# Optimization experiments

Measured on AMD Instinct MI355X. Metric: run time of the kernel, lower is better.

## Reference

```python
import jax, jax.numpy as jnp
import numpy as np
from jax import lax

# ---- configuration (matches init_kwargs / input_specs) ----
N = 16384          # number of input points
F_IN = 64          # input feature dim
RATIO = 0.25       # fps ratio
M = int(N * RATIO) # number of sampled centers = 4096
RADIUS = 0.2       # radius for neighbor search
K = 64             # max_num_neighbors
F_HID = 64
F_OUT = 128


def _glorot(key, shape):
    fan_in = shape[0]
    return jax.random.normal(key, shape, jnp.float32) / jnp.sqrt(jnp.float32(fan_in))


def setup_inputs() -> dict:
    key = jax.random.key(0)
    ks = jax.random.split(key, 6)
    x = jax.random.normal(ks[0], (N, F_IN), jnp.float32)
    pos = jax.random.normal(ks[1], (N, 3), jnp.float32)
    batch = jnp.zeros((N,), jnp.int32)  # single point cloud
    # PointNet++ SA conv MLP: [F_IN+3 -> 64 -> 64 -> 128]
    W1 = _glorot(ks[2], (F_IN + 3, F_HID))
    b1 = jnp.zeros((F_HID,), jnp.float32)
    W2 = _glorot(ks[3], (F_HID, F_HID))
    b2 = jnp.zeros((F_HID,), jnp.float32)
    W3 = _glorot(ks[4], (F_HID, F_OUT))
    b3 = jnp.zeros((F_OUT,), jnp.float32)
    return {"x": x, "pos": pos, "batch": batch,
            "W1": W1, "b1": b1, "W2": W2, "b2": b2, "W3": W3, "b3": b3}


def fps(pos, m):
    """Farthest point sampling: returns m indices into pos [N,3]."""
    n = pos.shape[0]

    def step(carry, _):
        min_d2, last = carry
        d2 = jnp.sum((pos - pos[last]) ** 2, axis=-1)   # [N]
        min_d2 = jnp.minimum(min_d2, d2)
        nxt = jnp.argmax(min_d2).astype(jnp.int32)
        return (min_d2, nxt), last

    init = (jnp.full((n,), jnp.inf, pos.dtype), jnp.int32(0))
    _, idx = lax.scan(step, init, None, length=m)
    return idx  # [m]


def radius_neighbors(pos, pos_s, batch, batch_s, r, k):
    """For each center, k nearest neighbors within radius r (same batch).
    Returns nbr indices [M,K] and validity mask [M,K]."""
    d2 = jnp.sum((pos_s[:, None, :] - pos[None, :, :]) ** 2, axis=-1)  # [M,N]
    ok = (batch_s[:, None] == batch[None, :]) & (d2 <= r * r)
    score = jnp.where(ok, d2, jnp.inf)
    neg_vals, nbr = lax.top_k(-score, k)                # smallest distances first
    valid = jnp.isfinite(neg_vals)
    return nbr, valid


def reference(x, pos, batch, W1, b1, W2, b2, W3, b3):
    idx = fps(pos, M)                   # [M]
    pos_s = pos[idx]                    # [M,3]
    batch_s = batch[idx]                # [M]
    nbr, valid = radius_neighbors(pos, pos_s, batch, batch_s, RADIUS, K)
    # gather neighbor features and relative positions
    rel = pos[nbr] - pos_s[:, None, :]                      # [M,K,3]
    h = jnp.concatenate([x[nbr], rel], axis=-1)             # [M,K,F_IN+3]
    # per-edge MLP (PointNetConv message)
    h = jax.nn.relu(h @ W1 + b1)
    h = jax.nn.relu(h @ W2 + b2)
    h = jax.nn.relu(h @ W3 + b3)                            # [M,K,F_OUT]
    # max aggregation over valid neighbors (center is always its own neighbor)
    h = jnp.where(valid[..., None], h, -jnp.inf)
    out = jnp.max(h, axis=1)                                # [M,F_OUT]
    return out, pos_s, batch_s
```

## Files before the change

### kernel.cpp

```cpp
#include <hip/hip_runtime.h>

#define N_PTS 16384
#define M_CTR 4096
#define K_NBR 64
#define F_OUT 128
#define CAP   256
#define FS    68
#define NCELL 4096
#define NBKT  512

__device__ __forceinline__ float d2_exact(float ax, float ay, float az,
                                          float bx, float by, float bz) {
  float dx = __fsub_rn(ax, bx);
  float dy = __fsub_rn(ay, by);
  float dz = __fsub_rn(az, bz);
  return __fadd_rn(__fadd_rn(__fmul_rn(dx, dx), __fmul_rn(dy, dy)),
                   __fmul_rn(dz, dz));
}

__device__ __forceinline__ float readlane_f(float v, int ln) {
  return __int_as_float(__builtin_amdgcn_readlane(__float_as_int(v), ln));
}

__device__ __forceinline__ unsigned long long wave_max_u64(unsigned long long v) {
  int lo = (int)(unsigned)v;
  int hi = (int)(unsigned)(v >> 32);
#define DPPSTEP64(ctrl, rm)                                                    \
  {                                                                            \
    int tlo = __builtin_amdgcn_update_dpp(lo, lo, ctrl, rm, 0xf, false);       \
    int thi = __builtin_amdgcn_update_dpp(hi, hi, ctrl, rm, 0xf, false);       \
    unsigned long long cur =                                                   \
        ((unsigned long long)(unsigned)hi << 32) | (unsigned)lo;               \
    unsigned long long oth =                                                   \
        ((unsigned long long)(unsigned)thi << 32) | (unsigned)tlo;             \
    if (oth > cur) { lo = tlo; hi = thi; }                                     \
  }
  DPPSTEP64(0x111, 0xf) DPPSTEP64(0x112, 0xf) DPPSTEP64(0x114, 0xf)
  DPPSTEP64(0x118, 0xf) DPPSTEP64(0x142, 0xa) DPPSTEP64(0x143, 0xc)
#undef DPPSTEP64
  const unsigned rlo = (unsigned)__builtin_amdgcn_readlane(lo, 63);
  const unsigned rhi = (unsigned)__builtin_amdgcn_readlane(hi, 63);
  return ((unsigned long long)rhi << 32) | rlo;
}

__device__ __forceinline__ unsigned long long bucket_bfly_max_u64(
    unsigned long long red) {
#define RORSTEP(ctrl)                                                          \
  {                                                                            \
    int lo = (int)(unsigned)red, hi = (int)(unsigned)(red >> 32);              \
    int tlo = __builtin_amdgcn_update_dpp(lo, lo, ctrl, 0xf, 0xf, false);      \
    int thi = __builtin_amdgcn_update_dpp(hi, hi, ctrl, 0xf, 0xf, false);      \
    unsigned long long o =                                                     \
        ((unsigned long long)(unsigned)thi << 32) | (unsigned)tlo;             \
    if (o > red) red = o;                                                      \
  }
  RORSTEP(0x121) RORSTEP(0x122) RORSTEP(0x124) RORSTEP(0x128)
#undef RORSTEP
  const unsigned olo = (unsigned)__shfl_xor((int)(unsigned)red, 16);
  const unsigned ohi = (unsigned)__shfl_xor((int)(unsigned)(red >> 32), 16);
  const unsigned long long o = ((unsigned long long)ohi << 32) | olo;
  return (o > red) ? o : red;
}

__global__ void __launch_bounds__(1024) prep_bbox_kernel(const float* __restrict__ pos,
                                                         float* __restrict__ bbox,
                                                         int* __restrict__ hist) {
  const int tid = threadIdx.x;
  __shared__ float sred[6][16];
  float mn[3] = {INFINITY, INFINITY, INFINITY};
  float mx[3] = {-INFINITY, -INFINITY, -INFINITY};
  for (int p = tid; p < N_PTS; p += 1024) {
#pragma unroll
    for (int d = 0; d < 3; ++d) {
      float v = pos[3 * p + d];
      mn[d] = fminf(mn[d], v);
      mx[d] = fmaxf(mx[d], v);
    }
  }
#pragma unroll
  for (int off = 32; off > 0; off >>= 1) {
#pragma unroll
    for (int d = 0; d < 3; ++d) {
      mn[d] = fminf(mn[d], __shfl_xor(mn[d], off));
      mx[d] = fmaxf(mx[d], __shfl_xor(mx[d], off));
    }
  }
  if ((tid & 63) == 0) {
    const int w = tid >> 6;
#pragma unroll
    for (int d = 0; d < 3; ++d) { sred[d][w] = mn[d]; sred[3 + d][w] = mx[d]; }
  }
  __syncthreads();
  if (tid == 0) {
#pragma unroll
    for (int d = 0; d < 3; ++d) {
      float a = sred[d][0], b = sred[3 + d][0];
      for (int w = 1; w < 16; ++w) { a = fminf(a, sred[d][w]); b = fmaxf(b, sred[3 + d][w]); }
      bbox[d] = a; bbox[3 + d] = b;
    }
  }
  for (int i = tid; i < NCELL; i += 1024) hist[i] = 0;
}

__device__ __forceinline__ int spread4(int v) {
  return (v & 1) | ((v & 2) << 2) | ((v & 4) << 4) | ((v & 8) << 6);
}

__global__ void __launch_bounds__(256) prep_cell_kernel(const float* __restrict__ pos,
                                                        const float* __restrict__ bbox,
                                                        int* __restrict__ cellid,
                                                        int* __restrict__ hist) {
  const int p = blockIdx.x * 256 + threadIdx.x;
  const float x = pos[3 * p], y = pos[3 * p + 1], z = pos[3 * p + 2];
  const float x0 = bbox[0], y0 = bbox[1], z0 = bbox[2];
  const float sx = 16.0f / fmaxf(bbox[3] - x0, 1e-20f);
  const float sy = 16.0f / fmaxf(bbox[4] - y0, 1e-20f);
  const float sz = 16.0f / fmaxf(bbox[5] - z0, 1e-20f);
  int cx = min(15, (int)((x - x0) * sx));
  int cy = min(15, (int)((y - y0) * sy));
  int cz = min(15, (int)((z - z0) * sz));
  const int c = spread4(cx) | (spread4(cy) << 1) | (spread4(cz) << 2);
  cellid[p] = c;
  atomicAdd(&hist[c], 1);
}

__global__ void __launch_bounds__(1024) prep_scan_kernel(const int* __restrict__ hist,
                                                         int* __restrict__ cursor) {
  __shared__ int tsum[1024];
  const int t = threadIdx.x;
  const int v0 = hist[4 * t + 0], v1 = hist[4 * t + 1];
  const int v2 = hist[4 * t + 2], v3 = hist[4 * t + 3];
  const int s = v0 + v1 + v2 + v3;
  int acc = s;
  tsum[t] = acc;
  __syncthreads();
  for (int off = 1; off < 1024; off <<= 1) {
    int add = (t >= off) ? tsum[t - off] : 0;
    __syncthreads();
    acc += add;
    tsum[t] = acc;
    __syncthreads();
  }
  int base = acc - s;
  cursor[4 * t + 0] = base;
  cursor[4 * t + 1] = base + v0;
  cursor[4 * t + 2] = base + v0 + v1;
  cursor[4 * t + 3] = base + v0 + v1 + v2;
}

__global__ void __launch_bounds__(256) prep_scatter_kernel(const float* __restrict__ pos,
                                                           const int* __restrict__ cellid,
                                                           int* __restrict__ cursor,
                                                           float4* __restrict__ gxyz) {
  const int p = blockIdx.x * 256 + threadIdx.x;
  const int c = cellid[p];
  const int dst = atomicAdd(&cursor[c], 1);
  gxyz[dst] = make_float4(pos[3 * p + 0], pos[3 * p + 1], pos[3 * p + 2],
                          __int_as_float(p));
}

__global__ void __launch_bounds__(64) prep_bktbox_kernel(const float4* __restrict__ gxyz,
                                                         float* __restrict__ gbox) {
  const int lane = threadIdx.x;
  const float4 q = gxyz[blockIdx.x * 64 + lane];
  float mnx = q.x, mxx = q.x, mny = q.y, mxy = q.y, mnz = q.z, mxz = q.z;
#pragma unroll
  for (int off = 16; off > 0; off >>= 1) {
    mnx = fminf(mnx, __shfl_xor(mnx, off)); mxx = fmaxf(mxx, __shfl_xor(mxx, off));
    mny = fminf(mny, __shfl_xor(mny, off)); mxy = fmaxf(mxy, __shfl_xor(mxy, off));
    mnz = fminf(mnz, __shfl_xor(mnz, off)); mxz = fmaxf(mxz, __shfl_xor(mxz, off));
  }
  if ((lane & 31) == 0) {
    const int b = blockIdx.x * 2 + (lane >> 5);
    gbox[b * 8 + 0] = mnx; gbox[b * 8 + 1] = mxx;
    gbox[b * 8 + 2] = mny; gbox[b * 8 + 3] = mxy;
    gbox[b * 8 + 4] = mnz; gbox[b * 8 + 5] = mxz;
    gbox[b * 8 + 6] = 0.0f; gbox[b * 8 + 7] = 0.0f;
  }
}

__global__ void __launch_bounds__(512) fps_bucket_kernel(
    const float* __restrict__ pos, const float4* __restrict__ gxyz,
    const float* __restrict__ gbox,
    int* __restrict__ idx_out, float* __restrict__ pos_s_out,
    float* __restrict__ batch_s_out) {
  __shared__ float s_md[N_PTS];
  __shared__ unsigned long long s_pk[NBKT];
  __shared__ float4 s_wxyz[NBKT];
  __shared__ int s_wl[NBKT];
  __shared__ int s_cnt[2];
  __shared__ int s_sidx[M_CTR];
  const int tid = threadIdx.x;
  const int lane = tid & 63, wave = tid >> 6;

  for (int i = tid; i < N_PTS; i += 512) s_md[i] = INFINITY;
  const float bx0 = gbox[tid * 8 + 0], bx1 = gbox[tid * 8 + 1];
  const float by0 = gbox[tid * 8 + 2], by1 = gbox[tid * 8 + 3];
  const float bz0 = gbox[tid * 8 + 4], bz1 = gbox[tid * 8 + 5];
  unsigned long long mpk = ((unsigned long long)0x7f800000u << 32);
  s_pk[tid] = mpk;
  if (tid < 2) s_cnt[tid] = 0;

  float cxA = pos[0], cyA = pos[1], czA = pos[2];
  int idA = 0;
  float cxB = 0.0f, cyB = 0.0f, czB = 0.0f;
  int idB = 0;
  bool dual = false;
  int t = 0, rc = 0;
  __syncthreads();

  while (true) {
    if (tid == 0) s_sidx[t] = idA;
    ++t;
    if (t >= M_CTR) break;
    if (dual) {
      if (tid == 0) s_sidx[t] = idB;
      ++t;
      if (t >= M_CTR) break;
    }
    const int par = rc & 1;
    ++rc;

    const float rMax = __uint_as_float((unsigned)(mpk >> 32));
    float dxl = fmaxf(fmaxf(bx0 - cxA, cxA - bx1), 0.0f);
    float dyl = fmaxf(fmaxf(by0 - cyA, cyA - by1), 0.0f);
    float dzl = fmaxf(fmaxf(bz0 - czA, czA - bz1), 0.0f);
    bool flag = (dxl * dxl + dyl * dyl + dzl * dzl) * 0.99999f < rMax;
    if (dual) {
      float ex = fmaxf(fmaxf(bx0 - cxB, cxB - bx1), 0.0f);
      float ey = fmaxf(fmaxf(by0 - cyB, cyB - by1), 0.0f);
      float ez = fmaxf(fmaxf(bz0 - czB, czB - bz1), 0.0f);
      flag = flag || ((ex * ex + ey * ey + ez * ez) * 0.99999f < rMax);
    }
    const unsigned long long ball = __ballot(flag);
    int base = 0;
    if (lane == 0) base = atomicAdd(&s_cnt[par], __popcll(ball));
    base = __builtin_amdgcn_readfirstlane(base);
    if (flag) {
      const int pre = __popcll(ball & ((1ull << lane) - 1ull));
      s_wl[base + pre] = tid;
    }
    __syncthreads();
    if (tid == 0) s_cnt[par ^ 1] = 0;

    const int nf = s_cnt[par];
    const int total = nf << 5;
    for (int bi = 0; bi < total; bi += 512) {
      const int idx = bi + tid;
      if (idx < total) {
        const int b = s_wl[idx >> 5];
        const int p = (b << 5) | (idx & 31);
        const float4 q = gxyz[p];
        float nmd = fminf(s_md[p], d2_exact(q.x, q.y, q.z, cxA, cyA, czA));
        if (dual) nmd = fminf(nmd, d2_exact(q.x, q.y, q.z, cxB, cyB, czB));
        s_md[p] = nmd;
        const unsigned long long own =
            ((unsigned long long)__float_as_uint(nmd) << 32) |
            ((unsigned long long)(16383u - (unsigned)__float_as_int(q.w)) << 14) |
            (unsigned)p;
        const unsigned long long red = bucket_bfly_max_u64(own);
        if (own == red) {
          s_pk[b] = red;
          s_wxyz[b] = make_float4(q.x, q.y, q.z, 0.0f);
        }
      }
    }
    __syncthreads();

    unsigned long long vv[8];
    unsigned long long loc = 0ULL;
#pragma unroll
    for (int k = 0; k < 8; ++k) {
      const unsigned long long u = s_pk[(k << 6) | lane];
      vv[k] = u;
      if (k == wave) mpk = u;
      if (u > loc) loc = u;
    }
    const unsigned long long bpk = wave_max_u64(loc);
    idA = 16383 - (int)((bpk >> 14) & 16383u);
    const int posn1 = (int)(bpk & 16383u);
    const int b1 = posn1 >> 5;
    {
      const float4 cq = s_wxyz[b1];
      cxA = cq.x; cyA = cq.y; czA = cq.z;
    }

    unsigned long long loc2 = 0ULL;
#pragma unroll
    for (int k = 0; k < 8; ++k) {
      const int bb = (k << 6) | lane;
      const unsigned long long u = (bb == b1) ? 0ULL : vv[k];
      if (u > loc2) loc2 = u;
    }
    const int pp = (b1 << 5) | (lane & 31);
    const float mdv = s_md[pp];
    const float4 qq = gxyz[pp];
    unsigned long long spk =
        ((unsigned long long)__float_as_uint(mdv) << 32) |
        ((unsigned long long)(16383u - (unsigned)__float_as_int(qq.w)) << 14) |
        (unsigned)pp;
    if (pp == posn1) spk = 0ULL;
    if (spk > loc2) loc2 = spk;
    const unsigned long long Rpk = wave_max_u64(loc2);
    const unsigned hiR = (unsigned)(Rpk >> 32);
    const int posnR = (int)(Rpk & 16383u);
    float rx, ry, rz;
    if ((posnR >> 5) == b1) {
      const int ln = posnR & 31;
      rx = readlane_f(qq.x, ln);
      ry = readlane_f(qq.y, ln);
      rz = readlane_f(qq.z, ln);
    } else {
      const float4 w = s_wxyz[posnR >> 5];
      rx = w.x; ry = w.y; rz = w.z;
    }
    const float dAR = d2_exact(rx, ry, rz, cxA, cyA, czA);
    dual = (hiR != 0u) && (dAR >= __uint_as_float(hiR));
    if (dual) {
      cxB = rx; cyB = ry; czB = rz;
      idB = 16383 - (int)((Rpk >> 14) & 16383u);
    }
  }
  __syncthreads();
  for (int i = tid; i < M_CTR; i += 512) {
    const int si = s_sidx[i];
    idx_out[i] = si;
    pos_s_out[3 * i + 0] = pos[3 * si + 0];
    pos_s_out[3 * i + 1] = pos[3 * si + 1];
    pos_s_out[3 * i + 2] = pos[3 * si + 2];
    batch_s_out[i] = 0.0f;
  }
}

__global__ void __launch_bounds__(256) nbr_kernel(const float* __restrict__ pos,
                                                  const int* __restrict__ idx,
                                                  int* __restrict__ nbr) {
  const int m = blockIdx.x, tid = threadIdx.x;
  __shared__ int s_cnt;
  __shared__ float s_d2[CAP];
  __shared__ int s_idx[CAP];
  if (tid == 0) s_cnt = 0;
  const int cen = idx[m];
  const float cx = pos[3 * cen + 0], cy = pos[3 * cen + 1], cz = pos[3 * cen + 2];
  __syncthreads();
  const float RR = 0.04f;
  for (int i = 0; i < N_PTS / 256; ++i) {
    const int p = tid + 256 * i;
    float d2 = d2_exact(pos[3 * p], pos[3 * p + 1], pos[3 * p + 2], cx, cy, cz);
    if (d2 <= RR) {
      int slot = atomicAdd(&s_cnt, 1);
      if (slot < CAP) { s_d2[slot] = d2; s_idx[slot] = p; }
    }
  }
  __syncthreads();
  const int cnt = s_cnt;
  if (cnt <= K_NBR) {
    if (tid < K_NBR) nbr[m * K_NBR + tid] = (tid < cnt) ? s_idx[tid] : cen;
  } else {
    const int n = cnt < CAP ? cnt : CAP;
    if (tid >= n) { s_d2[tid] = INFINITY; s_idx[tid] = 0x7fffffff; }
    __syncthreads();
    for (int k = 2; k <= CAP; k <<= 1) {
      for (int j = k >> 1; j > 0; j >>= 1) {
        const int ixj = tid ^ j;
        if (ixj > tid) {
          float da = s_d2[tid], db = s_d2[ixj];
          int ia = s_idx[tid], ib = s_idx[ixj];
          bool gt = (da > db) || (da == db && ia > ib);
          bool asc = ((tid & k) == 0);
          if (gt == asc) {
            s_d2[tid] = db; s_d2[ixj] = da;
            s_idx[tid] = ib; s_idx[ixj] = ia;
          }
        }
        __syncthreads();
      }
    }
    if (tid < K_NBR) nbr[m * K_NBR + tid] = s_idx[tid];
  }
}

__device__ __forceinline__ void mlp_layer(const float (*__restrict__ A)[FS],
                                          const float (*__restrict__ W)[64],
                                          int K, int e0, int c0, float acc[4][4]) {
#pragma unroll
  for (int j = 0; j < 4; ++j)
#pragma unroll
    for (int i = 0; i < 4; ++i) acc[j][i] = W[67][c0 + i];
#pragma unroll 4
  for (int k = 0; k < K; ++k) {
    const float4 w = *(const float4*)&W[k][c0];
    const float a0 = A[e0 + 0][k], a1 = A[e0 + 1][k];
    const float a2 = A[e0 + 2][k], a3 = A[e0 + 3][k];
    acc[0][0] = fmaf(a0, w.x, acc[0][0]); acc[0][1] = fmaf(a0, w.y, acc[0][1]);
    acc[0][2] = fmaf(a0, w.z, acc[0][2]); acc[0][3] = fmaf(a0, w.w, acc[0][3]);
    acc[1][0] = fmaf(a1, w.x, acc[1][0]); acc[1][1] = fmaf(a1, w.y, acc[1][1]);
    acc[1][2] = fmaf(a1, w.z, acc[1][2]); acc[1][3] = fmaf(a1, w.w, acc[1][3]);
    acc[2][0] = fmaf(a2, w.x, acc[2][0]); acc[2][1] = fmaf(a2, w.y, acc[2][1]);
    acc[2][2] = fmaf(a2, w.z, acc[2][2]); acc[2][3] = fmaf(a2, w.w, acc[2][3]);
    acc[3][0] = fmaf(a3, w.x, acc[3][0]); acc[3][1] = fmaf(a3, w.y, acc[3][1]);
    acc[3][2] = fmaf(a3, w.z, acc[3][2]); acc[3][3] = fmaf(a3, w.w, acc[3][3]);
  }
#pragma unroll
  for (int j = 0; j < 4; ++j)
#pragma unroll
    for (int i = 0; i < 4; ++i) acc[j][i] = fmaxf(acc[j][i], 0.0f);
}

__global__ void __launch_bounds__(512) mlp_kernel(
    const float* __restrict__ x, const float* __restrict__ pos,
    const int* __restrict__ nbr, const float* __restrict__ pos_s,
    const float* __restrict__ W1, const float* __restrict__ b1,
    const float* __restrict__ W2, const float* __restrict__ b2,
    const float* __restrict__ W3, const float* __restrict__ b3,
    float* __restrict__ out) {
  __shared__ float Fb[2][64][FS];
  __shared__ float Wb[FS][64];
  __shared__ float Pb[2][16][64];
  __shared__ int s_nbr[128];
  const int t = threadIdx.x;
  const int m0 = blockIdx.x * 2;

  if (t < 128) s_nbr[t] = nbr[m0 * K_NBR + t];
  __syncthreads();

  {
    const int ge = t >> 2, wch = ge >> 6, e = ge & 63, c16 = (t & 3) * 16;
    const int n = s_nbr[ge];
    const float4* src = (const float4*)(x + n * 64 + c16);
    float4* dst = (float4*)(&Fb[wch][e][c16]);
    dst[0] = src[0]; dst[1] = src[1]; dst[2] = src[2]; dst[3] = src[3];
  }
  if (t < 128) {
    const int wch = t >> 6, e = t & 63;
    const int n = s_nbr[t];
    const float cx = pos_s[(m0 + wch) * 3 + 0];
    const float cy = pos_s[(m0 + wch) * 3 + 1];
    const float cz = pos_s[(m0 + wch) * 3 + 2];
    Fb[wch][e][64] = pos[3 * n + 0] - cx;
    Fb[wch][e][65] = pos[3 * n + 1] - cy;
    Fb[wch][e][66] = pos[3 * n + 2] - cz;
    Fb[wch][e][67] = 0.0f;
  }
  for (int i = t; i < 67 * 64; i += 512) ((float*)Wb)[i] = W1[i];
  if (t < 64) Wb[67][t] = b1[t];
  __syncthreads();

  const int wch = t >> 8, tt = t & 255;
  const int e0 = (tt >> 4) << 2, c0 = (tt & 15) << 2;
  float acc[4][4];

  mlp_layer(Fb[wch], Wb, 67, e0, c0, acc);
  __syncthreads();
#pragma unroll
  for (int j = 0; j < 4; ++j)
#pragma unroll
    for (int i = 0; i < 4; ++i) Fb[wch][e0 + j][c0 + i] = acc[j][i];
  for (int i = t; i < 64 * 64; i += 512) ((float*)Wb)[i] = W2[i];
  if (t < 64) Wb[67][t] = b2[t];
  __syncthreads();

  mlp_layer(Fb[wch], Wb, 64, e0, c0, acc);
  __syncthreads();
#pragma unroll
  for (int j = 0; j < 4; ++j)
#pragma unroll
    for (int i = 0; i < 4; ++i) Fb[wch][e0 + j][c0 + i] = acc[j][i];

  for (int h = 0; h < 2; ++h) {
    for (int i = t; i < 64 * 64; i += 512)
      ((float*)Wb)[i] = W3[(i >> 6) * 128 + h * 64 + (i & 63)];
    if (t < 64) Wb[67][t] = b3[h * 64 + t];
    __syncthreads();
    mlp_layer(Fb[wch], Wb, 64, e0, c0, acc);
#pragma unroll
    for (int i = 0; i < 4; ++i) {
      float v = fmaxf(fmaxf(acc[0][i], acc[1][i]), fmaxf(acc[2][i], acc[3][i]));
      Pb[wch][tt >> 4][c0 + i] = v;
    }
    __syncthreads();
    if (tt < 64) {
      float v = Pb[wch][0][tt];
#pragma unroll
      for (int r = 1; r < 16; ++r) v = fmaxf(v, Pb[wch][r][tt]);
      out[(m0 + wch) * F_OUT + h * 64 + tt] = v;
    }
    __syncthreads();
  }
}

extern "C" void kernel_launch(void* const* d_in, const int* in_sizes, int n_in,
                              void* d_out, int out_size, void* d_ws, size_t ws_size,
                              hipStream_t stream) {
  const float* x   = (const float*)d_in[0];
  const float* pos = (const float*)d_in[1];
  const float* W1 = (const float*)d_in[3];
  const float* b1 = (const float*)d_in[4];
  const float* W2 = (const float*)d_in[5];
  const float* b2 = (const float*)d_in[6];
  const float* W3 = (const float*)d_in[7];
  const float* b3 = (const float*)d_in[8];

  float* out     = (float*)d_out;
  float* pos_s   = out + M_CTR * F_OUT;
  float* batch_s = pos_s + M_CTR * 3;

  int*    idx    = (int*)d_ws;
  int*    nbr    = idx + M_CTR;
  float*  bbox   = (float*)(nbr + M_CTR * K_NBR);
  int*    hist   = (int*)(bbox + 8);
  int*    cursor = hist + NCELL;
  int*    cellid = cursor + NCELL;
  float4* gxyz   = (float4*)(cellid + N_PTS);
  float*  gbox   = (float*)hist;

  prep_bbox_kernel<<<1, 1024, 0, stream>>>(pos, bbox, hist);
  prep_cell_kernel<<<N_PTS / 256, 256, 0, stream>>>(pos, bbox, cellid, hist);
  prep_scan_kernel<<<1, 1024, 0, stream>>>(hist, cursor);
  prep_scatter_kernel<<<N_PTS / 256, 256, 0, stream>>>(pos, cellid, cursor, gxyz);
  prep_bktbox_kernel<<<NBKT / 2, 64, 0, stream>>>(gxyz, gbox);
  fps_bucket_kernel<<<1, 512, 0, stream>>>(pos, gxyz, gbox, idx, pos_s, batch_s);
  nbr_kernel<<<M_CTR, 256, 0, stream>>>(pos, idx, nbr);
  mlp_kernel<<<M_CTR / 2, 512, 0, stream>>>(x, pos, nbr, pos_s,
                                            W1, b1, W2, b2, W3, b3, out);
}
```

Before: 5.376 ms.

## Halve FPS block to 256 threads and track per-bucket second max

The single-block FPS kernel drops from 512 to 256 threads, so each thread owns two buckets. This is meant to cut barrier and cross-wave overhead in the serial sequential loop. Each bucket now also records its second-largest packed distance and that point's coordinates during the update pass. The runner-up candidate then comes from this stored value instead of rescanning the winning bucket from s_md and gxyz. The cost is an extra butterfly reduction per updated point, more shared memory, and half the threads for the update loop.

```diff
diff --git a/kernel.cpp b/kernel.cpp
--- a/kernel.cpp
+++ b/kernel.cpp
@@ -16,10 +16,6 @@
   float dz = __fsub_rn(az, bz);
   return __fadd_rn(__fadd_rn(__fmul_rn(dx, dx), __fmul_rn(dy, dy)),
                    __fmul_rn(dz, dz));
-}
-
-__device__ __forceinline__ float readlane_f(float v, int ln) {
-  return __int_as_float(__builtin_amdgcn_readlane(__float_as_int(v), ln));
 }
 
 __device__ __forceinline__ unsigned long long wave_max_u64(unsigned long long v) {
@@ -179,26 +175,33 @@
   }
 }
 
-__global__ void __launch_bounds__(512) fps_bucket_kernel(
+__global__ void __launch_bounds__(256) fps_bucket_kernel(
     const float* __restrict__ pos, const float4* __restrict__ gxyz,
     const float* __restrict__ gbox,
     int* __restrict__ idx_out, float* __restrict__ pos_s_out,
     float* __restrict__ batch_s_out) {
   __shared__ float s_md[N_PTS];
   __shared__ unsigned long long s_pk[NBKT];
+  __shared__ unsigned long long s_pk2[NBKT];
   __shared__ float4 s_wxyz[NBKT];
+  __shared__ float4 s_wxyz2[NBKT];
   __shared__ int s_wl[NBKT];
   __shared__ int s_cnt[2];
   __shared__ int s_sidx[M_CTR];
   const int tid = threadIdx.x;
   const int lane = tid & 63, wave = tid >> 6;
-
-  for (int i = tid; i < N_PTS; i += 512) s_md[i] = INFINITY;
-  const float bx0 = gbox[tid * 8 + 0], bx1 = gbox[tid * 8 + 1];
-  const float by0 = gbox[tid * 8 + 2], by1 = gbox[tid * 8 + 3];
-  const float bz0 = gbox[tid * 8 + 4], bz1 = gbox[tid * 8 + 5];
-  unsigned long long mpk = ((unsigned long long)0x7f800000u << 32);
-  s_pk[tid] = mpk;
+  const int bA = tid, bB = tid + 256;
+
+  for (int i = tid; i < N_PTS; i += 256) s_md[i] = INFINITY;
+  const unsigned long long PKINF = ((unsigned long long)0x7f800000u << 32);
+  for (int i = tid; i < NBKT; i += 256) { s_pk[i] = PKINF; s_pk2[i] = 0ULL; }
+  const float aX0 = gbox[bA * 8 + 0], aX1 = gbox[bA * 8 + 1];
+  const float aY0 = gbox[bA * 8 + 2], aY1 = gbox[bA * 8 + 3];
+  const float aZ0 = gbox[bA * 8 + 4], aZ1 = gbox[bA * 8 + 5];
+  const float bX0 = gbox[bB * 8 + 0], bX1 = gbox[bB * 8 + 1];
+  const float bY0 = gbox[bB * 8 + 2], bY1 = gbox[bB * 8 + 3];
+  const float bZ0 = gbox[bB * 8 + 4], bZ1 = gbox[bB * 8 + 5];
+  unsigned long long mpkA = PKINF, mpkB = PKINF;
   if (tid < 2) s_cnt[tid] = 0;
 
   float cxA = pos[0], cyA = pos[1], czA = pos[2];
@@ -221,31 +224,47 @@
     const int par = rc & 1;
     ++rc;
 
-    const float rMax = __uint_as_float((unsigned)(mpk >> 32));
-    float dxl = fmaxf(fmaxf(bx0 - cxA, cxA - bx1), 0.0f);
-    float dyl = fmaxf(fmaxf(by0 - cyA, cyA - by1), 0.0f);
-    float dzl = fmaxf(fmaxf(bz0 - czA, czA - bz1), 0.0f);
-    bool flag = (dxl * dxl + dyl * dyl + dzl * dzl) * 0.99999f < rMax;
+    const float rMaxA = __uint_as_float((unsigned)(mpkA >> 32));
+    const float rMaxB = __uint_as_float((unsigned)(mpkB >> 32));
+    float d0, d1, d2v;
+    d0 = fmaxf(fmaxf(aX0 - cxA, cxA - aX1), 0.0f);
+    d1 = fmaxf(fmaxf(aY0 - cyA, cyA - aY1), 0.0f);
+    d2v = fmaxf(fmaxf(aZ0 - czA, czA - aZ1), 0.0f);
+    bool flagA = (d0 * d0 + d1 * d1 + d2v * d2v) * 0.99999f < rMaxA;
+    d0 = fmaxf(fmaxf(bX0 - cxA, cxA - bX1), 0.0f);
+    d1 = fmaxf(fmaxf(bY0 - cyA, cyA - bY1), 0.0f);
+    d2v = fmaxf(fmaxf(bZ0 - czA, czA - bZ1), 0.0f);
+    bool flagB = (d0 * d0 + d1 * d1 + d2v * d2v) * 0.99999f < rMaxB;
     if (dual) {
-      float ex = fmaxf(fmaxf(bx0 - cxB, cxB - bx1), 0.0f);
-      float ey = fmaxf(fmaxf(by0 - cyB, cyB - by1), 0.0f);
-      float ez = fmaxf(fmaxf(bz0 - czB, czB - bz1), 0.0f);
-      flag = flag || ((ex * ex + ey * ey + ez * ez) * 0.99999f < rMax);
-    }
-    const unsigned long long ball = __ballot(flag);
-    int base = 0;
-    if (lane == 0) base = atomicAdd(&s_cnt[par], __popcll(ball));
-    base = __builtin_amdgcn_readfirstlane(base);
-    if (flag) {
-      const int pre = __popcll(ball & ((1ull << lane) - 1ull));
-      s_wl[base + pre] = tid;
+      d0 = fmaxf(fmaxf(aX0 - cxB, cxB - aX1), 0.0f);
+      d1 = fmaxf(fmaxf(aY0 - cyB, cyB - aY1), 0.0f);
+      d2v = fmaxf(fmaxf(aZ0 - czB, czB - aZ1), 0.0f);
+      flagA = flagA || ((d0 * d0 + d1 * d1 + d2v * d2v) * 0.99999f < rMaxA);
+      d0 = fmaxf(fmaxf(bX0 - cxB, cxB - bX1), 0.0f);
+      d1 = fmaxf(fmaxf(bY0 - cyB, cyB - bY1), 0.0f);
+      d2v = fmaxf(fmaxf(bZ0 - czB, czB - bZ1), 0.0f);
+      flagB = flagB || ((d0 * d0 + d1 * d1 + d2v * d2v) * 0.99999f < rMaxB);
+    }
+    {
+      const unsigned long long ball = __ballot(flagA);
+      int base = 0;
+      if (lane == 0) base = atomicAdd(&s_cnt[par], __popcll(ball));
+      base = __builtin_amdgcn_readfirstlane(base);
+      if (flagA) s_wl[base + __popcll(ball & ((1ull << lane) - 1ull))] = bA;
+    }
+    {
+      const unsigned long long ball = __ballot(flagB);
+      int base = 0;
+      if (lane == 0) base = atomicAdd(&s_cnt[par], __popcll(ball));
+      base = __builtin_amdgcn_readfirstlane(base);
+      if (flagB) s_wl[base + __popcll(ball & ((1ull << lane) - 1ull))] = bB;
     }
     __syncthreads();
     if (tid == 0) s_cnt[par ^ 1] = 0;
 
     const int nf = s_cnt[par];
     const int total = nf << 5;
-    for (int bi = 0; bi < total; bi += 512) {
+    for (int bi = 0; bi < total; bi += 256) {
       const int idx = bi + tid;
       if (idx < total) {
         const int b = s_wl[idx >> 5];
@@ -258,11 +277,17 @@
             ((unsigned long long)__float_as_uint(nmd) << 32) |
             ((unsigned long long)(16383u - (unsigned)__float_as_int(q.w)) << 14) |
             (unsigned)p;
-        const unsigned long long red = bucket_bfly_max_u64(own);
-        if (own == red) {
-          s_pk[b] = red;
+        const unsigned long long r1 = bucket_bfly_max_u64(own);
+        const unsigned long long msk = (own == r1) ? 0ULL : own;
+        const unsigned long long r2 = bucket_bfly_max_u64(msk);
+        if (own == r1) {
+          s_pk[b] = r1;
+          s_pk2[b] = r2;
           s_wxyz[b] = make_float4(q.x, q.y, q.z, 0.0f);
         }
+        if (own == r2) {
+          s_wxyz2[b] = make_float4(q.x, q.y, q.z, 0.0f);
+        }
       }
     }
     __syncthreads();
@@ -271,45 +296,36 @@
     unsigned long long loc = 0ULL;
 #pragma unroll
     for (int k = 0; k < 8; ++k) {
-      const unsigned long long u = s_pk[(k << 6) | lane];
-      vv[k] = u;
-      if (k == wave) mpk = u;
-      if (u > loc) loc = u;
-    }
-    const unsigned long long bpk = wave_max_u64(loc);
-    idA = 16383 - (int)((bpk >> 14) & 16383u);
-    const int posn1 = (int)(bpk & 16383u);
+      vv[k] = s_pk[(k << 6) | lane];
+      if (vv[k] > loc) loc = vv[k];
+    }
+    const unsigned long long m1 = wave_max_u64(loc);
+    idA = 16383 - (int)((m1 >> 14) & 16383u);
+    const int posn1 = (int)(m1 & 16383u);
     const int b1 = posn1 >> 5;
     {
       const float4 cq = s_wxyz[b1];
       cxA = cq.x; cyA = cq.y; czA = cq.z;
     }
-
+    if (wave == 0)      { mpkA = vv[0]; mpkB = vv[4]; }
+    else if (wave == 1) { mpkA = vv[1]; mpkB = vv[5]; }
+    else if (wave == 2) { mpkA = vv[2]; mpkB = vv[6]; }
+    else                { mpkA = vv[3]; mpkB = vv[7]; }
     unsigned long long loc2 = 0ULL;
 #pragma unroll
     for (int k = 0; k < 8; ++k) {
-      const int bb = (k << 6) | lane;
-      const unsigned long long u = (bb == b1) ? 0ULL : vv[k];
+      const unsigned long long u = (vv[k] == m1) ? 0ULL : vv[k];
       if (u > loc2) loc2 = u;
     }
-    const int pp = (b1 << 5) | (lane & 31);
-    const float mdv = s_md[pp];
-    const float4 qq = gxyz[pp];
-    unsigned long long spk =
-        ((unsigned long long)__float_as_uint(mdv) << 32) |
-        ((unsigned long long)(16383u - (unsigned)__float_as_int(qq.w)) << 14) |
-        (unsigned)pp;
-    if (pp == posn1) spk = 0ULL;
-    if (spk > loc2) loc2 = spk;
-    const unsigned long long Rpk = wave_max_u64(loc2);
+    unsigned long long Rpk = wave_max_u64(loc2);
+    const unsigned long long pk2b1 = s_pk2[b1];
+    if (pk2b1 > Rpk) Rpk = pk2b1;
     const unsigned hiR = (unsigned)(Rpk >> 32);
     const int posnR = (int)(Rpk & 16383u);
     float rx, ry, rz;
     if ((posnR >> 5) == b1) {
-      const int ln = posnR & 31;
-      rx = readlane_f(qq.x, ln);
-      ry = readlane_f(qq.y, ln);
-      rz = readlane_f(qq.z, ln);
+      const float4 w = s_wxyz2[b1];
+      rx = w.x; ry = w.y; rz = w.z;
     } else {
       const float4 w = s_wxyz[posnR >> 5];
       rx = w.x; ry = w.y; rz = w.z;
@@ -322,7 +338,7 @@
     }
   }
   __syncthreads();
-  for (int i = tid; i < M_CTR; i += 512) {
+  for (int i = tid; i < M_CTR; i += 256) {
     const int si = s_sidx[i];
     idx_out[i] = si;
     pos_s_out[3 * i + 0] = pos[3 * si + 0];
@@ -519,7 +535,7 @@
   prep_scan_kernel<<<1, 1024, 0, stream>>>(hist, cursor);
   prep_scatter_kernel<<<N_PTS / 256, 256, 0, stream>>>(pos, cellid, cursor, gxyz);
   prep_bktbox_kernel<<<NBKT / 2, 64, 0, stream>>>(gxyz, gbox);
-  fps_bucket_kernel<<<1, 512, 0, stream>>>(pos, gxyz, gbox, idx, pos_s, batch_s);
+  fps_bucket_kernel<<<1, 256, 0, stream>>>(pos, gxyz, gbox, idx, pos_s, batch_s);
   nbr_kernel<<<M_CTR, 256, 0, stream>>>(pos, idx, nbr);
   mlp_kernel<<<M_CTR / 2, 512, 0, stream>>>(x, pos, nbr, pos_s,
                                             W1, b1, W2, b2, W3, b3, out);
```

New measurement: 8.594 ms. +59.9%, slower.
